# Kernel optimization log

Hardware: AMD Instinct MI355X
Metric: run time of the kernel (lower is better)

## Reference

```python
import jax, jax.numpy as jnp
import numpy as np

# Contiguous token segment lengths per group (static, sums to 4096)
LEN_GROUPS = (256, 512, 768, 384, 640, 512, 576, 448)
NUM_GROUPS, D_IN, D_OUT = 8, 512, 512
BATCH = 16


def setup_inputs() -> dict:
    key = jax.random.key(0)
    k1, k2, k3 = jax.random.split(key, 3)
    T = int(sum(LEN_GROUPS))
    x = jax.random.normal(k1, (BATCH, T, D_IN), dtype=jnp.float32)
    # nn.Linear default init: U(-1/sqrt(fan_in), 1/sqrt(fan_in))
    bound = 1.0 / np.sqrt(D_IN)
    W = jax.random.uniform(k2, (NUM_GROUPS, D_OUT, D_IN), jnp.float32, -bound, bound)
    b = jax.random.uniform(k3, (NUM_GROUPS, D_OUT), jnp.float32, -bound, bound)
    return {"x": x, "W": W, "b": b}


def reference(x, W, b):
    # Per-group Linear over contiguous token segments, then concat along tokens.
    # Loop is over a small static group count; segment bounds are Python ints,
    # so slicing is static and jit-compatible.
    outs = []
    start = 0
    for i, L in enumerate(LEN_GROUPS):
        seg = x[:, start:start + L]                     # [B, L, D_in]
        outs.append(jnp.einsum('btd,od->bto', seg, W[i]) + b[i])  # [B, L, D_out]
        start += L
    return jnp.concatenate(outs, axis=1)               # [B, T, D_out]
```

## Files before the change

### kernel.cpp

```cpp
#include <hip/hip_runtime.h>
#include <hip/hip_bf16.h>
#include <cstdint>

#define BATCH 16
#define TTOT  4096
#define DIN   512
#define DOUT  512
#define NG    8
#define NKT   8

typedef float f32x4 __attribute__((ext_vector_type(4)));
typedef short s16x8 __attribute__((ext_vector_type(8)));

__device__ __forceinline__ short f2b(float f) {
    union { __bf16 b; short s; } u; u.b = (__bf16)f; return u.s;
}

__global__ void wconv_kernel(const float* __restrict__ W, ushort* __restrict__ wbf) {
    int gid = blockIdx.x * 256 + threadIdx.x;
    int c = gid >> 12;
    int q = (gid & 4095) << 4;
    int row = q >> 7;
    int bc  = q & 127;
    int k = ((c & 7) << 6) + ((bc ^ ((row & 7) << 4)) >> 1);
    int g = c >> 3;
    const float* wp = W + ((size_t)((g << 9) + row) << 9) + k;
    float4 v0 = *reinterpret_cast<const float4*>(wp);
    float4 v1 = *reinterpret_cast<const float4*>(wp + 4);
    s16x8 o;
    o[0]=f2b(v0.x); o[1]=f2b(v0.y); o[2]=f2b(v0.z); o[3]=f2b(v0.w);
    o[4]=f2b(v1.x); o[5]=f2b(v1.y); o[6]=f2b(v1.z); o[7]=f2b(v1.w);
    *reinterpret_cast<s16x8*>((char*)wbf + (size_t)c * 65536 + q) = o;
}

__launch_bounds__(512, 2)
__global__ void gemm_kernel(const float* __restrict__ x,
                            const ushort* __restrict__ wbf,
                            const float* __restrict__ bias,
                            float* __restrict__ out) {
    __shared__ __align__(16) char smem[147456];

    const int tid  = threadIdx.x;
    const int lane = tid & 63;
    const int wv   = tid >> 6;
    const int colf = lane & 15;
    const int kg   = lane >> 4;

    const int p  = blockIdx.x;
    const int l  = ((p & 7) << 7) + (p >> 3);
    const int mt = l >> 4;
    const int batch = l & 15;
    const int t0 = mt << 6;
    int g = 0;
    if (mt >= 4)  g++; if (mt >= 12) g++; if (mt >= 24) g++;
    if (mt >= 30) g++; if (mt >= 40) g++; if (mt >= 48) g++;
    if (mt >= 57) g++;

    const char* bchunk = (const char*)wbf + (size_t)(g << 3) * 65536;

    const int arow = tid >> 3;
    const int koff = ((tid & 7) ^ (arow & 7)) << 3;
    const float* aptr = x + ((size_t)((batch << 12) + t0 + arow) << 9) + koff;
    const int awb = (arow << 7) + ((tid & 7) << 4);

    float4 aE[2], aO[2];
    f32x4 acc[4][4];
#pragma unroll
    for (int mi = 0; mi < 4; ++mi)
#pragma unroll
        for (int ni = 0; ni < 4; ++ni)
            acc[mi][ni] = (f32x4){0.f, 0.f, 0.f, 0.f};

#define ISSUE_A(S, KT_) do {                                                \
        const float* p_ = aptr + ((KT_) << 6);                              \
        a##S[0] = *(const float4*)(p_);                                     \
        a##S[1] = *(const float4*)(p_ + 4);                                 \
    } while (0)

#define CVT_WRITE_A(S, KT_) do {                                            \
        s16x8 o_;                                                           \
        o_[0]=f2b(a##S[0].x); o_[1]=f2b(a##S[0].y);                         \
        o_[2]=f2b(a##S[0].z); o_[3]=f2b(a##S[0].w);                         \
        o_[4]=f2b(a##S[1].x); o_[5]=f2b(a##S[1].y);                         \
        o_[6]=f2b(a##S[1].z); o_[7]=f2b(a##S[1].w);                         \
        *(s16x8*)(smem + (((KT_) & 1) << 13) + awb) = o_;                   \
    } while (0)

#define ISSUE_B(KT_) do {                                                   \
        const char* s_ = bchunk + ((size_t)(KT_) << 16) + tid * 16;         \
        char* d_ = smem + 16384 + (((KT_) & 1) << 16) + tid * 16;           \
        _Pragma("unroll")                                                   \
        for (int i_ = 0; i_ < 8; ++i_) {                                    \
            __builtin_amdgcn_global_load_lds(                               \
                (const __attribute__((address_space(1))) void*)(s_ + i_ * 8192), \
                (__attribute__((address_space(3))) void*)(d_ + i_ * 8192),  \
                16, 0, 0);                                                  \
        }                                                                   \
    } while (0)

#define COMPUTE(KT_) do {                                                   \
        const char* ab_ = smem + (((KT_) & 1) << 13);                       \
        const char* bb_ = smem + 16384 + (((KT_) & 1) << 16);               \
        _Pragma("unroll")                                                   \
        for (int ks = 0; ks < 2; ++ks) {                                    \
            const int kb = ks * 64 + (kg << 4);                             \
            s16x8 af[4], bf[4];                                             \
            _Pragma("unroll")                                               \
            for (int mi = 0; mi < 4; ++mi) {                                \
                int r_ = mi * 16 + colf;                                    \
                af[mi] = *(const s16x8*)(ab_ + (r_ << 7) + (kb ^ ((r_ & 7) << 4))); \
            }                                                               \
            _Pragma("unroll")                                               \
            for (int ni = 0; ni < 4; ++ni) {                                \
                int r_ = (wv << 6) + ni * 16 + colf;                        \
                bf[ni] = *(const s16x8*)(bb_ + (r_ << 7) + (kb ^ ((r_ & 7) << 4))); \
            }                                                               \
            _Pragma("unroll")                                               \
            for (int mi = 0; mi < 4; ++mi)                                  \
                _Pragma("unroll")                                           \
                for (int ni = 0; ni < 4; ++ni)                              \
                    acc[mi][ni] = __builtin_amdgcn_mfma_f32_16x16x32_bf16(  \
                        af[mi], bf[ni], acc[mi][ni], 0, 0, 0);              \
        }                                                                   \
    } while (0)

#define FENCE  asm volatile("" ::: "memory")
#define WAITV2 asm volatile("s_waitcnt vmcnt(2)" ::: "memory")
#define WAITV0 asm volatile("s_waitcnt vmcnt(0)" ::: "memory")
#define WAITL0 asm volatile("s_waitcnt lgkmcnt(0)" ::: "memory")
#define BAR    __builtin_amdgcn_s_barrier()

    ISSUE_A(E, 0);
    FENCE;
    ISSUE_B(0);
    FENCE;
    ISSUE_A(O, 1);
    FENCE;
    CVT_WRITE_A(E, 0);
    WAITV2;
    WAITL0;
    BAR;

#pragma unroll
    for (int kt = 0; kt < NKT; ++kt) {
        if (kt + 1 < NKT) { ISSUE_B(kt + 1); FENCE; }
        if (kt + 2 < NKT) {
            if (((kt + 2) & 1) == 0) { ISSUE_A(E, kt + 2); }
            else                     { ISSUE_A(O, kt + 2); }
            FENCE;
        }
        COMPUTE(kt);
        if (kt + 1 < NKT) {
            if (((kt + 1) & 1) == 0) { CVT_WRITE_A(E, kt + 1); }
            else                     { CVT_WRITE_A(O, kt + 1); }
            if (kt + 2 < NKT) { WAITV2; }
            else              { WAITV0; }
            WAITL0;
            BAR;
        }
    }
    BAR;

    float* cbuf = (float*)smem;
#pragma unroll
    for (int mi = 0; mi < 4; ++mi)
#pragma unroll
        for (int ni = 0; ni < 4; ++ni) {
            const int r0 = mi * 16 + kg * 4;
            const int c  = (wv << 6) + ni * 16 + colf;
            f32x4 v = acc[mi][ni];
            cbuf[(r0 + 0) * 516 + c] = v[0];
            cbuf[(r0 + 1) * 516 + c] = v[1];
            cbuf[(r0 + 2) * 516 + c] = v[2];
            cbuf[(r0 + 3) * 516 + c] = v[3];
        }
    WAITL0;
    BAR;

    const int rr = tid >> 3;
    const int c0 = (tid & 7) << 6;
    float* orow = out + ((size_t)((batch << 12) + t0 + rr) << 9) + c0;
    const float* crow = cbuf + rr * 516 + c0;
    const float* brow = bias + (g << 9) + c0;
#pragma unroll
    for (int i = 0; i < 16; ++i) {
        float4 v  = *(const float4*)(crow + (i << 2));
        float4 bv = *(const float4*)(brow + (i << 2));
        float4 o4;
        o4.x = v.x + bv.x; o4.y = v.y + bv.y;
        o4.z = v.z + bv.z; o4.w = v.w + bv.w;
        *(float4*)(orow + (i << 2)) = o4;
    }
#undef ISSUE_A
#undef CVT_WRITE_A
#undef ISSUE_B
#undef COMPUTE
#undef FENCE
#undef WAITV2
#undef WAITV0
#undef WAITL0
#undef BAR
}

__launch_bounds__(256)
__global__ void gemm_fallback(const float* __restrict__ x,
                              const float* __restrict__ W,
                              const float* __restrict__ bias,
                              float* __restrict__ out) {
    __shared__ __align__(16) char smem[49152];
    const int tid  = threadIdx.x;
    const int lane = tid & 63;
    const int wid  = tid >> 6;
    const int wm   = wid >> 1;
    const int wn   = wid & 1;
    const int p  = blockIdx.x;
    const int l  = ((p & 7) << 9) + (p >> 3);
    const int mt = l >> 2;
    const int nt = l & 3;
    const int bb = mt >> 6;
    const int t0 = (mt & 63) << 6;
    const int n0 = nt << 7;
    int g = 0;
    if (t0 >= 256)  g++; if (t0 >= 768)  g++; if (t0 >= 1536) g++;
    if (t0 >= 1920) g++; if (t0 >= 2560) g++; if (t0 >= 3072) g++;
    if (t0 >= 3648) g++;
    const int arow = tid >> 2;
    const int acol = (tid & 3) << 4;
    const float* aptr = x + ((size_t)(bb * TTOT + t0 + arow)) * DIN + acol;
    float4 a0, a1, a2, a3;
    float4 bw0[4], bw1[4];
    auto load_global = [&](int k0) {
        a0 = *(const float4*)(aptr + k0);
        a1 = *(const float4*)(aptr + k0 + 4);
        a2 = *(const float4*)(aptr + k0 + 8);
        a3 = *(const float4*)(aptr + k0 + 12);
#pragma unroll
        for (int pp = 0; pp < 4; ++pp) {
            int idx = pp * 256 + tid;
            int row = idx >> 3, seg = idx & 7;
            const float* wp = W + ((size_t)((g << 9) + n0 + row)) * DIN + k0 + (seg << 3);
            bw0[pp] = *(const float4*)(wp);
            bw1[pp] = *(const float4*)(wp + 4);
        }
    };
    auto swzf = [](int row, int bc) { return (row << 7) + (bc ^ ((row & 7) << 4)); };
    auto write_lds = [&](int buf) {
        char* ab  = smem + buf * 8192;
        char* bb_ = smem + 16384 + buf * 16384;
        s16x8 w0, w1;
        w0[0]=f2b(a0.x); w0[1]=f2b(a0.y); w0[2]=f2b(a0.z); w0[3]=f2b(a0.w);
        w0[4]=f2b(a1.x); w0[5]=f2b(a1.y); w0[6]=f2b(a1.z); w0[7]=f2b(a1.w);
        w1[0]=f2b(a2.x); w1[1]=f2b(a2.y); w1[2]=f2b(a2.z); w1[3]=f2b(a2.w);
        w1[4]=f2b(a3.x); w1[5]=f2b(a3.y); w1[6]=f2b(a3.z); w1[7]=f2b(a3.w);
        const int abase2 = acol << 1;
        *(s16x8*)(ab + swzf(arow, abase2))      = w0;
        *(s16x8*)(ab + swzf(arow, abase2 + 16)) = w1;
#pragma unroll
        for (int pp = 0; pp < 4; ++pp) {
            int idx = pp * 256 + tid;
            int row = idx >> 3, seg = idx & 7;
            s16x8 wvv;
            wvv[0]=f2b(bw0[pp].x); wvv[1]=f2b(bw0[pp].y);
            wvv[2]=f2b(bw0[pp].z); wvv[3]=f2b(bw0[pp].w);
            wvv[4]=f2b(bw1[pp].x); wvv[5]=f2b(bw1[pp].y);
            wvv[6]=f2b(bw1[pp].z); wvv[7]=f2b(bw1[pp].w);
            *(s16x8*)(bb_ + swzf(row, seg << 4)) = wvv;
        }
    };
    f32x4 acc[2][4];
#pragma unroll
    for (int mi = 0; mi < 2; ++mi)
#pragma unroll
        for (int ni = 0; ni < 4; ++ni) acc[mi][ni] = (f32x4){0.f,0.f,0.f,0.f};
    const int colf = lane & 15;
    const int kgrp = lane >> 4;
    auto compute = [&](int buf) {
        const char* ab  = smem + buf * 8192;
        const char* bb_ = smem + 16384 + buf * 16384;
#pragma unroll
        for (int ks = 0; ks < 2; ++ks) {
            const int kb = ks * 64 + kgrp * 16;
            s16x8 af[2], bf[4];
#pragma unroll
            for (int mi = 0; mi < 2; ++mi)
                af[mi] = *(const s16x8*)(ab + swzf(wm * 32 + mi * 16 + colf, kb));
#pragma unroll
            for (int ni = 0; ni < 4; ++ni)
                bf[ni] = *(const s16x8*)(bb_ + swzf(wn * 64 + ni * 16 + colf, kb));
#pragma unroll
            for (int mi = 0; mi < 2; ++mi)
#pragma unroll
                for (int ni = 0; ni < 4; ++ni)
                    acc[mi][ni] = __builtin_amdgcn_mfma_f32_16x16x32_bf16(
                        af[mi], bf[ni], acc[mi][ni], 0, 0, 0);
        }
    };
    load_global(0);
    write_lds(0);
    __syncthreads();
    int buf = 0;
#pragma unroll 1
    for (int kt = 0; kt < 8; ++kt) {
        if (kt < 7) load_global((kt + 1) << 6);
        compute(buf);
        if (kt < 7) write_lds(buf ^ 1);
        __syncthreads();
        buf ^= 1;
    }
    float* cbuf = (float*)smem;
#pragma unroll
    for (int ni = 0; ni < 4; ++ni) {
        const int c = wn * 64 + ni * 16 + colf;
#pragma unroll
        for (int mi = 0; mi < 2; ++mi) {
            const int rr2 = wm * 32 + mi * 16 + kgrp * 4;
            f32x4 v = acc[mi][ni];
            cbuf[(rr2 + 0) * 132 + c] = v[0];
            cbuf[(rr2 + 1) * 132 + c] = v[1];
            cbuf[(rr2 + 2) * 132 + c] = v[2];
            cbuf[(rr2 + 3) * 132 + c] = v[3];
        }
    }
    __syncthreads();
    const int rr = tid >> 5;
    const int cc = (tid & 31) << 2;
    const float4 bvv = *(const float4*)(bias + (g << 9) + n0 + cc);
#pragma unroll
    for (int it = 0; it < 8; ++it) {
        const int row = it * 8 + rr;
        float4 v = *(const float4*)(cbuf + row * 132 + cc);
        float4 o4; o4.x = v.x + bvv.x; o4.y = v.y + bvv.y;
                   o4.z = v.z + bvv.z; o4.w = v.w + bvv.w;
        *(float4*)(out + ((size_t)(bb * TTOT) + t0 + row) * DOUT + n0 + cc) = o4;
    }
}

extern "C" void kernel_launch(void* const* d_in, const int* in_sizes, int n_in,
                              void* d_out, int out_size, void* d_ws, size_t ws_size,
                              hipStream_t stream) {
    const float* x    = (const float*)d_in[0];
    const float* W    = (const float*)d_in[1];
    const float* bias = (const float*)d_in[2];
    float* out = (float*)d_out;

    const size_t wbytes = (size_t)NG * DOUT * DIN * sizeof(ushort);

    if (ws_size >= wbytes) {
        ushort* wbf = (ushort*)d_ws;
        wconv_kernel<<<1024, 256, 0, stream>>>(W, wbf);
        gemm_kernel<<<1024, 512, 0, stream>>>(x, wbf, bias, out);
    } else {
        gemm_fallback<<<BATCH * 64 * 4, 256, 0, stream>>>(x, W, bias, out);
    }
}
```

Before: 116.5 us.

## Retile grouped GEMM to 128x128 blocks with job table and smaller LDS

Replaces the 64x512 tile (512 threads, 144KB LDS) with 128-row by 128-col tiles using 256 threads and 32KB LDS, driven by a constant job table that maps token segments to groups (with 64-row partial jobs at group boundaries). Weights are repacked into 128x32 K-slices with a new swizzle, K is stepped in 32-wide chunks over 16 iterations, and MFMA sections are wrapped in setprio. The epilogue stages output through LDS in four 32-row passes. The aim is higher occupancy and better A/B reuse per tile, at the cost of more barriers per K step and some wasted work in the partial-row jobs.

```diff
diff --git a/kernel.cpp b/kernel.cpp
--- a/kernel.cpp
+++ b/kernel.cpp
@@ -7,7 +7,8 @@
 #define DIN   512
 #define DOUT  512
 #define NG    8
-#define NKT   8
+#define NJOB  33
+#define NKT   16
 
 typedef float f32x4 __attribute__((ext_vector_type(4)));
 typedef short s16x8 __attribute__((ext_vector_type(8)));
@@ -16,119 +17,141 @@
     union { __bf16 b; short s; } u; u.b = (__bf16)f; return u.s;
 }
 
+__device__ __constant__ short JT0[NJOB] = {
+    0,128, 256,384,512,640, 768,896,1024,1152,1280,1408, 1536,1664,1792,
+    1920,2048,2176,2304,2432, 2560,2688,2816,2944, 3072,3200,3328,3456,
+    3584, 3648, 3712,3840,3968};
+__device__ __constant__ char JG[NJOB] = {
+    0,0, 1,1,1,1, 2,2,2,2,2,2, 3,3,3, 4,4,4,4,4, 5,5,5,5, 6,6,6,6, 6, 7, 7,7,7};
+__device__ __constant__ char JBM[NJOB] = {
+    127,127, 127,127,127,127, 127,127,127,127,127,127, 127,127,127,
+    127,127,127,127,127, 127,127,127,127, 127,127,127,127, 63, 63, 127,127,127};
+
 __global__ void wconv_kernel(const float* __restrict__ W, ushort* __restrict__ wbf) {
     int gid = blockIdx.x * 256 + threadIdx.x;
-    int c = gid >> 12;
-    int q = (gid & 4095) << 4;
-    int row = q >> 7;
-    int bc  = q & 127;
-    int k = ((c & 7) << 6) + ((bc ^ ((row & 7) << 4)) >> 1);
-    int g = c >> 3;
-    const float* wp = W + ((size_t)((g << 9) + row) << 9) + k;
+    int c = gid >> 9;
+    int q = (gid & 511) << 4;
+    int r = q >> 6;
+    int slot = (q >> 4) & 3;
+    int kt = c & 15, nt = (c >> 4) & 3, g = c >> 6;
+    int k = (kt << 5) + (((slot ^ ((r >> 1) & 3))) << 3);
+    const float* wp = W + ((size_t)((g << 9) + (nt << 7) + r) << 9) + k;
     float4 v0 = *reinterpret_cast<const float4*>(wp);
     float4 v1 = *reinterpret_cast<const float4*>(wp + 4);
     s16x8 o;
     o[0]=f2b(v0.x); o[1]=f2b(v0.y); o[2]=f2b(v0.z); o[3]=f2b(v0.w);
     o[4]=f2b(v1.x); o[5]=f2b(v1.y); o[6]=f2b(v1.z); o[7]=f2b(v1.w);
-    *reinterpret_cast<s16x8*>((char*)wbf + (size_t)c * 65536 + q) = o;
-}
-
-__launch_bounds__(512, 2)
+    *reinterpret_cast<s16x8*>((char*)wbf + (size_t)c * 8192 + q) = o;
+}
+
+__launch_bounds__(256, 4)
 __global__ void gemm_kernel(const float* __restrict__ x,
                             const ushort* __restrict__ wbf,
                             const float* __restrict__ bias,
                             float* __restrict__ out) {
-    __shared__ __align__(16) char smem[147456];
+    __shared__ __align__(16) char smem[32768];
 
     const int tid  = threadIdx.x;
     const int lane = tid & 63;
     const int wv   = tid >> 6;
+    const int wm   = wv >> 1;
+    const int wn   = wv & 1;
     const int colf = lane & 15;
     const int kg   = lane >> 4;
 
-    const int p  = blockIdx.x;
-    const int l  = ((p & 7) << 7) + (p >> 3);
-    const int mt = l >> 4;
-    const int batch = l & 15;
-    const int t0 = mt << 6;
-    int g = 0;
-    if (mt >= 4)  g++; if (mt >= 12) g++; if (mt >= 24) g++;
-    if (mt >= 30) g++; if (mt >= 40) g++; if (mt >= 48) g++;
-    if (mt >= 57) g++;
-
-    const char* bchunk = (const char*)wbf + (size_t)(g << 3) * 65536;
-
-    const int arow = tid >> 3;
-    const int koff = ((tid & 7) ^ (arow & 7)) << 3;
-    const float* aptr = x + ((size_t)((batch << 12) + t0 + arow) << 9) + koff;
-    const int awb = (arow << 7) + ((tid & 7) << 4);
-
-    float4 aE[2], aO[2];
-    f32x4 acc[4][4];
-#pragma unroll
-    for (int mi = 0; mi < 4; ++mi)
-#pragma unroll
-        for (int ni = 0; ni < 4; ++ni)
-            acc[mi][ni] = (f32x4){0.f, 0.f, 0.f, 0.f};
+    const int p    = blockIdx.x;
+    const int l    = (p & 7) * 264 + (p >> 3);
+    const int nt   = l & 3;
+    const int rest = l >> 2;
+    const int job  = rest >> 4;
+    const int bb   = rest & 15;
+    const int t0   = JT0[job];
+    const int g    = JG[job];
+    const int bmm1 = JBM[job];
+    const int n0   = nt << 7;
+
+    const char* bchunk = (const char*)wbf + ((size_t)(((g << 2) + nt) << 4)) * 8192;
+
+    const int r = tid >> 1;
+    const int h = tid & 1;
+    const int re = (r <= bmm1) ? r : bmm1;
+    const float* aptr = x + ((size_t)(bb * TTOT + t0 + re) << 9) + (h << 4);
+    const int sr = (r >> 1) & 3;
+    const int aw0 = (r << 6) + ((((h << 1) | 0) ^ sr) << 4);
+    const int aw1 = (r << 6) + ((((h << 1) | 1) ^ sr) << 4);
+
+    float4 aE[4], aO[4];
 
 #define ISSUE_A(S, KT_) do {                                                \
-        const float* p_ = aptr + ((KT_) << 6);                              \
+        const float* p_ = aptr + ((KT_) << 5);                              \
         a##S[0] = *(const float4*)(p_);                                     \
         a##S[1] = *(const float4*)(p_ + 4);                                 \
+        a##S[2] = *(const float4*)(p_ + 8);                                 \
+        a##S[3] = *(const float4*)(p_ + 12);                                \
     } while (0)
 
 #define CVT_WRITE_A(S, KT_) do {                                            \
-        s16x8 o_;                                                           \
-        o_[0]=f2b(a##S[0].x); o_[1]=f2b(a##S[0].y);                         \
-        o_[2]=f2b(a##S[0].z); o_[3]=f2b(a##S[0].w);                         \
-        o_[4]=f2b(a##S[1].x); o_[5]=f2b(a##S[1].y);                         \
-        o_[6]=f2b(a##S[1].z); o_[7]=f2b(a##S[1].w);                         \
-        *(s16x8*)(smem + (((KT_) & 1) << 13) + awb) = o_;                   \
+        char* ab_ = smem + (((KT_) & 1) << 13);                             \
+        s16x8 o0_, o1_;                                                     \
+        o0_[0]=f2b(a##S[0].x); o0_[1]=f2b(a##S[0].y);                       \
+        o0_[2]=f2b(a##S[0].z); o0_[3]=f2b(a##S[0].w);                       \
+        o0_[4]=f2b(a##S[1].x); o0_[5]=f2b(a##S[1].y);                       \
+        o0_[6]=f2b(a##S[1].z); o0_[7]=f2b(a##S[1].w);                       \
+        o1_[0]=f2b(a##S[2].x); o1_[1]=f2b(a##S[2].y);                       \
+        o1_[2]=f2b(a##S[2].z); o1_[3]=f2b(a##S[2].w);                       \
+        o1_[4]=f2b(a##S[3].x); o1_[5]=f2b(a##S[3].y);                       \
+        o1_[6]=f2b(a##S[3].z); o1_[7]=f2b(a##S[3].w);                       \
+        *(s16x8*)(ab_ + aw0) = o0_;                                         \
+        *(s16x8*)(ab_ + aw1) = o1_;                                         \
     } while (0)
 
 #define ISSUE_B(KT_) do {                                                   \
-        const char* s_ = bchunk + ((size_t)(KT_) << 16) + tid * 16;         \
-        char* d_ = smem + 16384 + (((KT_) & 1) << 16) + tid * 16;           \
-        _Pragma("unroll")                                                   \
-        for (int i_ = 0; i_ < 8; ++i_) {                                    \
-            __builtin_amdgcn_global_load_lds(                               \
-                (const __attribute__((address_space(1))) void*)(s_ + i_ * 8192), \
-                (__attribute__((address_space(3))) void*)(d_ + i_ * 8192),  \
-                16, 0, 0);                                                  \
-        }                                                                   \
+        const char* s_ = bchunk + ((size_t)(KT_) << 13) + tid * 16;         \
+        char* d_ = smem + 16384 + (((KT_) & 1) << 13) + tid * 16;           \
+        __builtin_amdgcn_global_load_lds(                                   \
+            (const __attribute__((address_space(1))) void*)(s_),            \
+            (__attribute__((address_space(3))) void*)(d_), 16, 0, 0);       \
+        __builtin_amdgcn_global_load_lds(                                   \
+            (const __attribute__((address_space(1))) void*)(s_ + 4096),     \
+            (__attribute__((address_space(3))) void*)(d_ + 4096), 16, 0, 0);\
     } while (0)
 
 #define COMPUTE(KT_) do {                                                   \
         const char* ab_ = smem + (((KT_) & 1) << 13);                       \
-        const char* bb_ = smem + 16384 + (((KT_) & 1) << 16);               \
+        const char* bb_ = smem + 16384 + (((KT_) & 1) << 13);               \
+        __builtin_amdgcn_s_setprio(1);                                      \
+        s16x8 bf[4];                                                        \
         _Pragma("unroll")                                                   \
-        for (int ks = 0; ks < 2; ++ks) {                                    \
-            const int kb = ks * 64 + (kg << 4);                             \
-            s16x8 af[4], bf[4];                                             \
+        for (int ni = 0; ni < 4; ++ni) {                                    \
+            int r_ = wn * 64 + ni * 16 + colf;                              \
+            bf[ni] = *(const s16x8*)(bb_ + (r_ << 6)                        \
+                        + (((kg ^ ((r_ >> 1) & 3))) << 4));                 \
+        }                                                                   \
+        _Pragma("unroll")                                                   \
+        for (int mi = 0; mi < 4; ++mi) {                                    \
+            int r_ = wm * 64 + mi * 16 + colf;                              \
+            s16x8 af = *(const s16x8*)(ab_ + (r_ << 6)                      \
+                        + (((kg ^ ((r_ >> 1) & 3))) << 4));                 \
             _Pragma("unroll")                                               \
-            for (int mi = 0; mi < 4; ++mi) {                                \
-                int r_ = mi * 16 + colf;                                    \
-                af[mi] = *(const s16x8*)(ab_ + (r_ << 7) + (kb ^ ((r_ & 7) << 4))); \
-            }                                                               \
-            _Pragma("unroll")                                               \
-            for (int ni = 0; ni < 4; ++ni) {                                \
-                int r_ = (wv << 6) + ni * 16 + colf;                        \
-                bf[ni] = *(const s16x8*)(bb_ + (r_ << 7) + (kb ^ ((r_ & 7) << 4))); \
-            }                                                               \
-            _Pragma("unroll")                                               \
-            for (int mi = 0; mi < 4; ++mi)                                  \
-                _Pragma("unroll")                                           \
-                for (int ni = 0; ni < 4; ++ni)                              \
-                    acc[mi][ni] = __builtin_amdgcn_mfma_f32_16x16x32_bf16(  \
-                        af[mi], bf[ni], acc[mi][ni], 0, 0, 0);              \
+            for (int ni = 0; ni < 4; ++ni)                                  \
+                acc[mi][ni] = __builtin_amdgcn_mfma_f32_16x16x32_bf16(      \
+                    af, bf[ni], acc[mi][ni], 0, 0, 0);                      \
         }                                                                   \
+        __builtin_amdgcn_s_setprio(0);                                      \
     } while (0)
 
 #define FENCE  asm volatile("" ::: "memory")
-#define WAITV2 asm volatile("s_waitcnt vmcnt(2)" ::: "memory")
+#define WAITV4 asm volatile("s_waitcnt vmcnt(4)" ::: "memory")
 #define WAITV0 asm volatile("s_waitcnt vmcnt(0)" ::: "memory")
 #define WAITL0 asm volatile("s_waitcnt lgkmcnt(0)" ::: "memory")
 #define BAR    __builtin_amdgcn_s_barrier()
+
+    f32x4 acc[4][4];
+#pragma unroll
+    for (int mi = 0; mi < 4; ++mi)
+#pragma unroll
+        for (int ni = 0; ni < 4; ++ni)
+            acc[mi][ni] = (f32x4){0.f, 0.f, 0.f, 0.f};
 
     ISSUE_A(E, 0);
     FENCE;
@@ -137,7 +160,7 @@
     ISSUE_A(O, 1);
     FENCE;
     CVT_WRITE_A(E, 0);
-    WAITV2;
+    WAITV4;
     WAITL0;
     BAR;
 
@@ -153,7 +176,7 @@
         if (kt + 1 < NKT) {
             if (((kt + 1) & 1) == 0) { CVT_WRITE_A(E, kt + 1); }
             else                     { CVT_WRITE_A(O, kt + 1); }
-            if (kt + 2 < NKT) { WAITV2; }
+            if (kt + 2 < NKT) { WAITV4; }
             else              { WAITV0; }
             WAITL0;
             BAR;
@@ -162,41 +185,53 @@
     BAR;
 
     float* cbuf = (float*)smem;
-#pragma unroll
-    for (int mi = 0; mi < 4; ++mi)
-#pragma unroll
-        for (int ni = 0; ni < 4; ++ni) {
-            const int r0 = mi * 16 + kg * 4;
-            const int c  = (wv << 6) + ni * 16 + colf;
-            f32x4 v = acc[mi][ni];
-            cbuf[(r0 + 0) * 516 + c] = v[0];
-            cbuf[(r0 + 1) * 516 + c] = v[1];
-            cbuf[(r0 + 2) * 516 + c] = v[2];
-            cbuf[(r0 + 3) * 516 + c] = v[3];
-        }
-    WAITL0;
-    BAR;
-
-    const int rr = tid >> 3;
-    const int c0 = (tid & 7) << 6;
-    float* orow = out + ((size_t)((batch << 12) + t0 + rr) << 9) + c0;
-    const float* crow = cbuf + rr * 516 + c0;
-    const float* brow = bias + (g << 9) + c0;
-#pragma unroll
-    for (int i = 0; i < 16; ++i) {
-        float4 v  = *(const float4*)(crow + (i << 2));
-        float4 bv = *(const float4*)(brow + (i << 2));
-        float4 o4;
-        o4.x = v.x + bv.x; o4.y = v.y + bv.y;
-        o4.z = v.z + bv.z; o4.w = v.w + bv.w;
-        *(float4*)(orow + (i << 2)) = o4;
+    const int er = tid >> 3;
+    const int ec = (tid & 7) << 4;
+    float4 bvv[4];
+#pragma unroll
+    for (int i = 0; i < 4; ++i)
+        bvv[i] = *(const float4*)(bias + (g << 9) + n0 + ec + (i << 2));
+
+#pragma unroll
+    for (int pp = 0; pp < 4; ++pp) {
+        if (wm == (pp >> 1)) {
+#pragma unroll
+            for (int m = 0; m < 2; ++m) {
+                const int mi = (pp & 1) * 2 + m;
+#pragma unroll
+                for (int ni = 0; ni < 4; ++ni) {
+                    const int base = (m * 16 + kg * 4) * 132 + wn * 64 + ni * 16 + colf;
+                    f32x4 v = acc[mi][ni];
+                    cbuf[base]       = v[0];
+                    cbuf[base + 132] = v[1];
+                    cbuf[base + 264] = v[2];
+                    cbuf[base + 396] = v[3];
+                }
+            }
+        }
+        WAITL0;
+        BAR;
+        const int row = pp * 32 + er;
+        if (row <= bmm1) {
+            float* orow = out + ((size_t)(bb * TTOT + t0 + row) << 9) + n0 + ec;
+            const float* crow = cbuf + er * 132 + ec;
+#pragma unroll
+            for (int i = 0; i < 4; ++i) {
+                float4 v = *(const float4*)(crow + (i << 2));
+                float4 o4;
+                o4.x = v.x + bvv[i].x; o4.y = v.y + bvv[i].y;
+                o4.z = v.z + bvv[i].z; o4.w = v.w + bvv[i].w;
+                *(float4*)(orow + (i << 2)) = o4;
+            }
+        }
+        BAR;
     }
 #undef ISSUE_A
 #undef CVT_WRITE_A
 #undef ISSUE_B
 #undef COMPUTE
 #undef FENCE
-#undef WAITV2
+#undef WAITV4
 #undef WAITV0
 #undef WAITL0
 #undef BAR
@@ -348,7 +383,7 @@
     if (ws_size >= wbytes) {
         ushort* wbf = (ushort*)d_ws;
         wconv_kernel<<<1024, 256, 0, stream>>>(W, wbf);
-        gemm_kernel<<<1024, 512, 0, stream>>>(x, wbf, bias, out);
+        gemm_kernel<<<NJOB * BATCH * 4, 256, 0, stream>>>(x, wbf, bias, out);
     } else {
         gemm_fallback<<<BATCH * 64 * 4, 256, 0, stream>>>(x, W, bias, out);
     }
```

Result: no change. 117.0 us (+0.4%).
